# Performance work log

Measured on AMD Instinct MI355X. Metric: run time of the kernel, lower is better.

## Reference

```python
import jax, jax.numpy as jnp
import numpy as np
import math

HEADS = 16
D = 1024
HEAD_DIM = D // HEADS
SEQ = 2048
BATCH = 4
LN_EPS = 1e-5


def setup_inputs() -> dict:
    key = jax.random.key(0)
    ks = jax.random.split(key, 7)
    s = 1.0 / math.sqrt(HEAD_DIM)
    return {
        "q": jax.random.normal(ks[0], (SEQ, BATCH, D), dtype=jnp.float32),
        "k": jax.random.normal(ks[1], (SEQ, BATCH, D), dtype=jnp.float32),
        "v": jax.random.normal(ks[2], (SEQ, BATCH, D), dtype=jnp.float32),
        "Wq": jax.random.normal(ks[3], (HEAD_DIM, HEAD_DIM), dtype=jnp.float32) * s,
        "Wk": jax.random.normal(ks[4], (HEAD_DIM, HEAD_DIM), dtype=jnp.float32) * s,
        "Wv": jax.random.normal(ks[5], (HEAD_DIM, HEAD_DIM), dtype=jnp.float32) * s,
        "Wl": jax.random.normal(ks[6], (D, D), dtype=jnp.float32) * (1.0 / math.sqrt(D)),
        "gamma": jnp.ones((D,), dtype=jnp.float32),
        "beta": jnp.zeros((D,), dtype=jnp.float32),
    }


def reference(q, k, v, Wq, Wk, Wv, Wl, gamma, beta):
    # q, k, v: [seq_len, batch, d]  (seq-first, as in the torch module)
    q_len, batch = q.shape[0], q.shape[1]
    k_len, v_len = k.shape[0], v.shape[0]
    # Faithful to torch: reshape (NOT transpose) seq-first tensor into
    # (batch, len, heads, head_dim), then per-head linear (x @ W.T, no bias).
    Qh = jnp.einsum('bqhd,ed->bqhe', q.reshape(batch, q_len, HEADS, HEAD_DIM), Wq)
    Kh = jnp.einsum('bkhd,ed->bkhe', k.reshape(batch, k_len, HEADS, HEAD_DIM), Wk)
    Vh = jnp.einsum('bvhd,ed->bvhe', v.reshape(batch, v_len, HEADS, HEAD_DIM), Wv)
    # Scores scaled by sqrt(d) (full model dim), as in the original.
    scores = jnp.einsum('bqhd,bkhd->bhqk', Qh, Kh) / math.sqrt(D)
    attn = jax.nn.softmax(scores, axis=-1)  # dropout p=0.0 -> identity
    out = jnp.einsum('bhqk,bkhd->bqhd', attn, Vh)  # [b, q, h, d]
    concat = out.reshape(q_len, batch, D)
    lin = concat @ Wl.T
    mean = jnp.mean(lin, axis=-1, keepdims=True)
    var = jnp.var(lin, axis=-1, keepdims=True)
    ln = (lin - mean) * jax.lax.rsqrt(var + LN_EPS) * gamma + beta
    return q + ln
```

## Files before the change

kernel.cpp:

```cpp
#include <hip/hip_runtime.h>

#define LOG2E 1.4426950408889634f

typedef __attribute__((ext_vector_type(8))) short short8_t;
typedef __attribute__((ext_vector_type(4))) float floatx4;
typedef __attribute__((ext_vector_type(16))) float floatx16;

#define MFMA(a,b,c)   __builtin_amdgcn_mfma_f32_16x16x32_bf16(a,b,c,0,0,0)
#define MFMA32(a,b,c) __builtin_amdgcn_mfma_f32_32x32x16_bf16(a,b,c,0,0,0)
#define GLOAD(g, l) __builtin_amdgcn_global_load_lds( \
    (const __attribute__((address_space(1))) unsigned int*)(g), \
    (__attribute__((address_space(3))) unsigned int*)(l), 16, 0, 0)

__device__ __forceinline__ unsigned short f2bf(float f){
    unsigned u = __float_as_uint(f);
    u = u + 0x7FFFu + ((u >> 16) & 1u);
    return (unsigned short)(u >> 16);
}
__device__ __forceinline__ float bf2f(unsigned short s){
    return __uint_as_float(((unsigned)s) << 16);
}
__device__ __forceinline__ unsigned cvtpk(float lo, float hi){
    unsigned r;
    asm("v_cvt_pk_bf16_f32 %0, %1, %2" : "=v"(r) : "v"(lo), "v"(hi));
    return r;
}
__device__ __forceinline__ void plswap(unsigned &a, unsigned &b){
    asm volatile("v_permlane32_swap_b32 %0, %1" : "+v"(a), "+v"(b));
}

union U8 { unsigned u[4]; short8_t s8; };

__global__ __launch_bounds__(256) void proj_kernel(
    const float* __restrict__ Xq, const float* __restrict__ Xk, const float* __restrict__ Xv,
    const float* __restrict__ Wq, const float* __restrict__ Wk, const float* __restrict__ Wv,
    unsigned short* __restrict__ qp, unsigned short* __restrict__ kp, unsigned short* __restrict__ vp)
{
    const int rt = blockIdx.x;
    const int h  = blockIdx.y;
    const int sel= blockIdx.z;
    const float* X = (sel==0)?Xq:(sel==1)?Xk:Xv;
    const float* W = (sel==0)?Wq:(sel==1)?Wk:Wv;
    unsigned short* O = (sel==0)?qp:(sel==1)?kp:vp;
    const float qs = (sel==0) ? ((1.0f/32.0f)*LOG2E) : 1.0f;

    const int t  = threadIdx.x;
    const int w  = t >> 6, l = t & 63;
    const int r5 = l & 31;
    const int hf = l >> 5;

    const int row0 = rt*128 + w*32;

    short8_t a[4];
    {
        const float* xb = X + (size_t)(row0 + r5)*1024 + h*64 + hf*8;
        #pragma unroll
        for (int kb=0; kb<4; kb++){
            float4 f0 = *reinterpret_cast<const float4*>(xb + kb*16);
            float4 f1 = *reinterpret_cast<const float4*>(xb + kb*16 + 4);
            U8 u;
            u.u[0] = cvtpk(f0.x, f0.y); u.u[1] = cvtpk(f0.z, f0.w);
            u.u[2] = cvtpk(f1.x, f1.y); u.u[3] = cvtpk(f1.z, f1.w);
            a[kb] = u.s8;
        }
    }
    short8_t b[2][4];
    #pragma unroll
    for (int nb=0; nb<2; nb++){
        const float* wb = W + (size_t)(nb*32 + r5)*64 + hf*8;
        #pragma unroll
        for (int kb=0; kb<4; kb++){
            float4 f0 = *reinterpret_cast<const float4*>(wb + kb*16);
            float4 f1 = *reinterpret_cast<const float4*>(wb + kb*16 + 4);
            U8 u;
            u.u[0] = cvtpk(f0.x, f0.y); u.u[1] = cvtpk(f0.z, f0.w);
            u.u[2] = cvtpk(f1.x, f1.y); u.u[3] = cvtpk(f1.z, f1.w);
            b[nb][kb] = u.s8;
        }
    }

    floatx16 acc[2] = {};
    #pragma unroll
    for (int nb=0; nb<2; nb++)
        #pragma unroll
        for (int kb=0; kb<4; kb++)
            acc[nb] = MFMA32(a[kb], b[nb][kb], acc[nb]);

    const int c   = rt >> 4;
    const size_t chbase = (size_t)(c*16 + h);

    #pragma unroll
    for (int nb=0; nb<2; nb++){
        const int e = nb*32 + r5;
        #pragma unroll
        for (int m=0; m<4; m++){
            unsigned p01 = cvtpk(acc[nb][4*m]*qs,   acc[nb][4*m+1]*qs);
            unsigned p23 = cvtpk(acc[nb][4*m+2]*qs, acc[nb][4*m+3]*qs);
            #pragma unroll
            for (int i=0; i<4; i++){
                unsigned short val = (unsigned short)
                    ((i==0)?p01 : (i==1)?(p01>>16) : (i==2)?p23 : (p23>>16));
                const int gr = row0 + i + 8*m + 4*hf;
                const int s  = gr & 2047;
                size_t addr;
                if (sel == 0){
                    addr = (chbase*2048 + s)*64 + e;
                } else {
                    const int kt_ = s >> 6, rl = s & 63;
                    const size_t tbase = (chbase*32 + kt_)*4096;
                    if (sel == 1)
                        addr = tbase + rl*64 + (((e>>3) ^ (rl&7))<<3) + (e&7);
                    else
                        addr = tbase + e*64 + (((rl>>3) ^ (e&7))<<3) + (rl&7);
                }
                O[addr] = val;
            }
        }
    }
}

__global__ __launch_bounds__(256) void attn_kernel(
    const unsigned short* __restrict__ qp, const unsigned short* __restrict__ kp,
    const unsigned short* __restrict__ vp, unsigned short* __restrict__ ob)
{
    const int qt = blockIdx.x;
    const int hd = blockIdx.y;
    const int c  = blockIdx.z;
    const int t  = threadIdx.x;
    const int w  = t >> 6, l = t & 63;
    const int r5 = l & 31;
    const int hf = l >> 5;

    __shared__ unsigned short Ks[2][64][64];
    __shared__ unsigned short Vs[2][64][64];

    const size_t chq = ((size_t)(c*16 + hd))*2048*64;
    const size_t cht = ((size_t)(c*16 + hd))*32*4096;

    short8_t aq[4];
    {
        const unsigned short* qrow = qp + chq + (size_t)(qt*128 + w*32 + r5)*64 + hf*8;
        #pragma unroll
        for (int kb=0;kb<4;kb++)
            aq[kb] = *reinterpret_cast<const short8_t*>(qrow + kb*16);
    }

    const char* kbase = (const char*)(kp + cht) + w*2048 + l*16;
    const char* vbase = (const char*)(vp + cht) + w*2048 + l*16;
    char* kdst = (char*)(&Ks[0][0][0]) + w*2048;
    char* vdst = (char*)(&Vs[0][0][0]) + w*2048;

    #define ATTN_STAGE(buf, kt) do { \
        const char* ks_ = kbase + (size_t)(kt)*8192; \
        const char* vs_ = vbase + (size_t)(kt)*8192; \
        char* kd_ = kdst + (buf)*8192; \
        char* vd_ = vdst + (buf)*8192; \
        GLOAD(ks_,      kd_);      GLOAD(ks_+1024, kd_+1024); \
        GLOAD(vs_,      vd_);      GLOAD(vs_+1024, vd_+1024); \
    } while(0)

    const int x7 = r5 & 7;

    floatx16 oa[2] = {};
    float ls = 0.f;

    ATTN_STAGE(0, 0);

    for (int kt=0; kt<32; kt++){
        const int cur = kt & 1;
        if (kt < 31){
            ATTN_STAGE(cur^1, kt+1);
            asm volatile("s_waitcnt vmcnt(4)" ::: "memory");
        } else {
            asm volatile("s_waitcnt vmcnt(0)" ::: "memory");
        }
        __builtin_amdgcn_s_barrier();
        __builtin_amdgcn_sched_barrier(0);

        const unsigned short* Kc = &Ks[cur][0][0];
        const unsigned short* Vc = &Vs[cur][0][0];

        floatx16 sacc[2] = {};
        __builtin_amdgcn_s_setprio(1);
        #pragma unroll
        for (int mb=0;mb<2;mb++){
            #pragma unroll
            for (int kb=0;kb<4;kb++){
                short8_t kf = *reinterpret_cast<const short8_t*>(
                    Kc + (mb*32 + r5)*64 + (((kb*2 + hf) ^ x7)<<3));
                sacc[mb] = MFMA32(kf, aq[kb], sacc[mb]);
            }
        }
        __builtin_amdgcn_s_setprio(0);

        #pragma unroll
        for (int mb=0;mb<2;mb++)
            #pragma unroll
            for (int i=0;i<16;i++)
                sacc[mb][i] = __builtin_amdgcn_exp2f(sacc[mb][i]);

        float rsx[16];
        #pragma unroll
        for (int i=0;i<16;i++) rsx[i] = sacc[0][i] + sacc[1][i];
        #pragma unroll
        for (int s=8;s>0;s>>=1){
            #pragma unroll
            for (int i=0;i<s;i++) rsx[i] += rsx[i+s];
        }
        ls += rsx[0];

        short8_t F[4];
        #pragma unroll
        for (int mb=0;mb<2;mb++){
            unsigned lo[4], hi[4];
            #pragma unroll
            for (int m=0;m<4;m++){
                lo[m] = cvtpk(sacc[mb][4*m],   sacc[mb][4*m+1]);
                hi[m] = cvtpk(sacc[mb][4*m+2], sacc[mb][4*m+3]);
            }
            #pragma unroll
            for (int hk=0;hk<2;hk++){
                unsigned a = lo[2*hk], b = lo[2*hk+1];
                unsigned cc = hi[2*hk], d = hi[2*hk+1];
                plswap(a, b);
                plswap(cc, d);
                U8 fu;
                fu.u[0] = a; fu.u[1] = cc; fu.u[2] = b; fu.u[3] = d;
                F[mb*2 + hk] = fu.s8;
            }
        }

        __builtin_amdgcn_s_setprio(1);
        #pragma unroll
        for (int db=0;db<2;db++){
            #pragma unroll
            for (int kb2=0;kb2<4;kb2++){
                short8_t vf = *reinterpret_cast<const short8_t*>(
                    Vc + (db*32 + r5)*64 + (((kb2*2 + hf) ^ x7)<<3));
                oa[db] = MFMA32(vf, F[kb2], oa[db]);
            }
        }
        __builtin_amdgcn_s_setprio(0);

        __builtin_amdgcn_sched_barrier(0);
        __builtin_amdgcn_s_barrier();
    }

    ls += __shfl_xor(ls, 32);
    const float inv = 1.0f / ls;
    const size_t grow = (size_t)c*2048 + qt*128 + w*32 + r5;
    unsigned short* obp = ob + grow*1024 + hd*64 + hf*4;
    #pragma unroll
    for (int db=0;db<2;db++){
        #pragma unroll
        for (int m=0;m<4;m++){
            ushort4 u;
            u.x = f2bf(oa[db][4*m]*inv);   u.y = f2bf(oa[db][4*m+1]*inv);
            u.z = f2bf(oa[db][4*m+2]*inv); u.w = f2bf(oa[db][4*m+3]*inv);
            *reinterpret_cast<ushort4*>(obp + db*32 + m*8) = u;
        }
    }
}

__global__ __launch_bounds__(256) void wlconv_kernel(const float* __restrict__ W,
                                                     unsigned short* __restrict__ O)
{
    int i = (blockIdx.x*256 + threadIdx.x)*4;
    float4 f = *reinterpret_cast<const float4*>(W + i);
    ushort4 u;
    u.x = f2bf(f.x); u.y = f2bf(f.y); u.z = f2bf(f.z); u.w = f2bf(f.w);
    *reinterpret_cast<ushort4*>(O + i) = u;
}

__global__ __launch_bounds__(256) void gemm_kernel(
    const unsigned short* __restrict__ A, const unsigned short* __restrict__ B,
    unsigned short* __restrict__ C)
{
    const int bm = blockIdx.x, bn = blockIdx.y;
    __shared__ unsigned short As[2][128][64];
    __shared__ unsigned short Bs[2][128][64];
    const int t = threadIdx.x, w = t>>6, l = t&63;
    const int l15 = l&15, l4 = l>>4;
    const int wm = w>>1, wn = w&1;

    const char* asrc = (const char*)A + ((size_t)(bm*128 + w*32 + (l>>3)))*2048 + (l&7)*16;
    const char* bsrc = (const char*)B + ((size_t)(bn*128 + w*32 + (l>>3)))*2048 + (l&7)*16;
    char* adst = (char*)(&As[0][0][0]) + w*4096;
    char* bdst = (char*)(&Bs[0][0][0]) + w*4096;

    #define GEMM_STAGE(buf, kt) do { \
        const char* as_ = asrc + (size_t)(kt)*128; \
        const char* bs_ = bsrc + (size_t)(kt)*128; \
        char* ad_ = adst + (buf)*16384; \
        char* bd_ = bdst + (buf)*16384; \
        GLOAD(as_,          ad_);        GLOAD(as_+16384,  ad_+1024); \
        GLOAD(as_+32768,    ad_+2048);   GLOAD(as_+49152,  ad_+3072); \
        GLOAD(bs_,          bd_);        GLOAD(bs_+16384,  bd_+1024); \
        GLOAD(bs_+32768,    bd_+2048);   GLOAD(bs_+49152,  bd_+3072); \
    } while(0)

    floatx4 acc[4][4] = {};

    GEMM_STAGE(0, 0);

    for (int kt=0; kt<16; kt++){
        const int cur = kt & 1;
        if (kt < 15){
            GEMM_STAGE(cur^1, kt+1);
            asm volatile("s_waitcnt vmcnt(8)" ::: "memory");
        } else {
            asm volatile("s_waitcnt vmcnt(0)" ::: "memory");
        }
        __builtin_amdgcn_s_barrier();
        __builtin_amdgcn_sched_barrier(0);

        #pragma unroll
        for (int kk=0;kk<2;kk++){
            short8_t a[4], b[4];
            #pragma unroll
            for (int mt=0;mt<4;mt++)
                a[mt] = *reinterpret_cast<const short8_t*>(&As[cur][wm*64 + mt*16 + l15][kk*32 + l4*8]);
            #pragma unroll
            for (int nt=0;nt<4;nt++)
                b[nt] = *reinterpret_cast<const short8_t*>(&Bs[cur][wn*64 + nt*16 + l15][kk*32 + l4*8]);
            __builtin_amdgcn_s_setprio(1);
            #pragma unroll
            for (int mt=0;mt<4;mt++)
                #pragma unroll
                for (int nt=0;nt<4;nt++)
                    acc[mt][nt] = MFMA(a[mt], b[nt], acc[mt][nt]);
            __builtin_amdgcn_s_setprio(0);
        }

        __builtin_amdgcn_sched_barrier(0);
        __builtin_amdgcn_s_barrier();
    }

    #pragma unroll
    for (int mt=0;mt<4;mt++)
        #pragma unroll
        for (int nt=0;nt<4;nt++)
            #pragma unroll
            for (int j=0;j<4;j++){
                int row = bm*128 + wm*64 + mt*16 + l4*4 + j;
                int col = bn*128 + wn*64 + nt*16 + l15;
                C[(size_t)row*1024 + col] = f2bf(acc[mt][nt][j]);
            }
}

__global__ __launch_bounds__(256) void ln_kernel(
    const unsigned short* __restrict__ lin, const float* __restrict__ qin,
    const float* __restrict__ gamma, const float* __restrict__ beta, float* __restrict__ out)
{
    const int r = blockIdx.x, t = threadIdx.x;
    const unsigned short* row = lin + (size_t)r*1024;
    uint2 u = *reinterpret_cast<const uint2*>(row + t*4);
    float v0 = bf2f((unsigned short)(u.x & 0xffffu));
    float v1 = bf2f((unsigned short)(u.x >> 16));
    float v2 = bf2f((unsigned short)(u.y & 0xffffu));
    float v3 = bf2f((unsigned short)(u.y >> 16));
    float s  = v0+v1+v2+v3;
    float sq = v0*v0+v1*v1+v2*v2+v3*v3;
    #pragma unroll
    for (int d=1; d<64; d<<=1){ s += __shfl_xor(s, d); sq += __shfl_xor(sq, d); }
    __shared__ float red[8];
    if ((t&63)==0){ red[(t>>6)*2] = s; red[(t>>6)*2+1] = sq; }
    __syncthreads();
    s  = red[0]+red[2]+red[4]+red[6];
    sq = red[1]+red[3]+red[5]+red[7];
    float mean = s*(1.f/1024.f);
    float var  = sq*(1.f/1024.f) - mean*mean;
    float rs   = rsqrtf(var + 1e-5f);
    int base = r*1024 + t*4;
    float4 qv = *reinterpret_cast<const float4*>(qin + base);
    float4 g  = *reinterpret_cast<const float4*>(gamma + t*4);
    float4 b  = *reinterpret_cast<const float4*>(beta + t*4);
    float4 o;
    o.x = qv.x + (v0-mean)*rs*g.x + b.x;
    o.y = qv.y + (v1-mean)*rs*g.y + b.y;
    o.z = qv.z + (v2-mean)*rs*g.z + b.z;
    o.w = qv.w + (v3-mean)*rs*g.w + b.w;
    *reinterpret_cast<float4*>(out + base) = o;
}

extern "C" void kernel_launch(void* const* d_in, const int* in_sizes, int n_in,
                              void* d_out, int out_size, void* d_ws, size_t ws_size,
                              hipStream_t stream)
{
    (void)in_sizes; (void)n_in; (void)out_size; (void)ws_size;
    const float* q     = (const float*)d_in[0];
    const float* k     = (const float*)d_in[1];
    const float* v     = (const float*)d_in[2];
    const float* Wq    = (const float*)d_in[3];
    const float* Wk    = (const float*)d_in[4];
    const float* Wv    = (const float*)d_in[5];
    const float* Wl    = (const float*)d_in[6];
    const float* gamma = (const float*)d_in[7];
    const float* beta  = (const float*)d_in[8];
    float* out = (float*)d_out;

    char* ws = (char*)d_ws;
    unsigned short* qp  = (unsigned short*)(ws);
    unsigned short* kp  = (unsigned short*)(ws + (16u<<20));
    unsigned short* vp  = (unsigned short*)(ws + (32u<<20));
    unsigned short* ob  = (unsigned short*)(ws + (48u<<20));
    unsigned short* lin = (unsigned short*)(ws);
    unsigned short* wlb = (unsigned short*)(ws + (16u<<20));

    proj_kernel <<<dim3(64,16,3),  256, 0, stream>>>(q,k,v, Wq,Wk,Wv, qp,kp,vp);
    attn_kernel <<<dim3(16,16,4),  256, 0, stream>>>(qp,kp,vp, ob);
    wlconv_kernel<<<dim3(1024),    256, 0, stream>>>(Wl, wlb);
    gemm_kernel <<<dim3(64,8),     256, 0, stream>>>(ob, wlb, lin);
    ln_kernel   <<<dim3(8192),     256, 0, stream>>>(lin, q, gamma, beta, out);
}
```

Baseline: 190.9 us.

## Process two query tiles per wave in attention and compute row sums via MFMA

Each attention wave now handles 64 query rows (two 32-row tiles) instead of 32, so every K/V fragment read from LDS feeds two MFMAs. The grid is halved to match. The softmax row-sum is now accumulated with an MFMA against a vector of bf16 ones instead of a VALU reduction tree. This raises register pressure (launch bounds set to 1 block) and halves the block count, which may reduce occupancy and latency hiding.

```diff
diff --git a/kernel.cpp b/kernel.cpp
--- a/kernel.cpp
+++ b/kernel.cpp
@@ -119,7 +119,7 @@
     }
 }
 
-__global__ __launch_bounds__(256) void attn_kernel(
+__global__ __launch_bounds__(256,1) void attn_kernel(
     const unsigned short* __restrict__ qp, const unsigned short* __restrict__ kp,
     const unsigned short* __restrict__ vp, unsigned short* __restrict__ ob)
 {
@@ -137,12 +137,15 @@
     const size_t chq = ((size_t)(c*16 + hd))*2048*64;
     const size_t cht = ((size_t)(c*16 + hd))*32*4096;
 
-    short8_t aq[4];
+    short8_t aqA[4], aqB[4];
     {
-        const unsigned short* qrow = qp + chq + (size_t)(qt*128 + w*32 + r5)*64 + hf*8;
-        #pragma unroll
-        for (int kb=0;kb<4;kb++)
-            aq[kb] = *reinterpret_cast<const short8_t*>(qrow + kb*16);
+        const unsigned short* qrowA = qp + chq + (size_t)(qt*256 + w*64 + r5)*64 + hf*8;
+        const unsigned short* qrowB = qrowA + 32*64;
+        #pragma unroll
+        for (int kb=0;kb<4;kb++){
+            aqA[kb] = *reinterpret_cast<const short8_t*>(qrowA + kb*16);
+            aqB[kb] = *reinterpret_cast<const short8_t*>(qrowB + kb*16);
+        }
     }
 
     const char* kbase = (const char*)(kp + cht) + w*2048 + l*16;
@@ -161,8 +164,13 @@
 
     const int x7 = r5 & 7;
 
-    floatx16 oa[2] = {};
-    float ls = 0.f;
+    U8 onesu;
+    onesu.u[0] = 0x3F803F80u; onesu.u[1] = 0x3F803F80u;
+    onesu.u[2] = 0x3F803F80u; onesu.u[3] = 0x3F803F80u;
+    const short8_t ones8 = onesu.s8;
+
+    floatx16 oaA[2] = {}, oaB[2] = {};
+    floatx16 lsA = {}, lsB = {};
 
     ATTN_STAGE(0, 0);
 
@@ -180,7 +188,7 @@
         const unsigned short* Kc = &Ks[cur][0][0];
         const unsigned short* Vc = &Vs[cur][0][0];
 
-        floatx16 sacc[2] = {};
+        floatx16 sA[2] = {}, sB[2] = {};
         __builtin_amdgcn_s_setprio(1);
         #pragma unroll
         for (int mb=0;mb<2;mb++){
@@ -188,35 +196,26 @@
             for (int kb=0;kb<4;kb++){
                 short8_t kf = *reinterpret_cast<const short8_t*>(
                     Kc + (mb*32 + r5)*64 + (((kb*2 + hf) ^ x7)<<3));
-                sacc[mb] = MFMA32(kf, aq[kb], sacc[mb]);
+                sA[mb] = MFMA32(kf, aqA[kb], sA[mb]);
+                sB[mb] = MFMA32(kf, aqB[kb], sB[mb]);
             }
         }
         __builtin_amdgcn_s_setprio(0);
 
+        short8_t FA[4], FB[4];
+
         #pragma unroll
         for (int mb=0;mb<2;mb++)
             #pragma unroll
             for (int i=0;i<16;i++)
-                sacc[mb][i] = __builtin_amdgcn_exp2f(sacc[mb][i]);
-
-        float rsx[16];
-        #pragma unroll
-        for (int i=0;i<16;i++) rsx[i] = sacc[0][i] + sacc[1][i];
-        #pragma unroll
-        for (int s=8;s>0;s>>=1){
-            #pragma unroll
-            for (int i=0;i<s;i++) rsx[i] += rsx[i+s];
-        }
-        ls += rsx[0];
-
-        short8_t F[4];
+                sA[mb][i] = __builtin_amdgcn_exp2f(sA[mb][i]);
         #pragma unroll
         for (int mb=0;mb<2;mb++){
             unsigned lo[4], hi[4];
             #pragma unroll
             for (int m=0;m<4;m++){
-                lo[m] = cvtpk(sacc[mb][4*m],   sacc[mb][4*m+1]);
-                hi[m] = cvtpk(sacc[mb][4*m+2], sacc[mb][4*m+3]);
+                lo[m] = cvtpk(sA[mb][4*m],   sA[mb][4*m+1]);
+                hi[m] = cvtpk(sA[mb][4*m+2], sA[mb][4*m+3]);
             }
             #pragma unroll
             for (int hk=0;hk<2;hk++){
@@ -226,9 +225,38 @@
                 plswap(cc, d);
                 U8 fu;
                 fu.u[0] = a; fu.u[1] = cc; fu.u[2] = b; fu.u[3] = d;
-                F[mb*2 + hk] = fu.s8;
-            }
-        }
+                FA[mb*2 + hk] = fu.s8;
+            }
+        }
+        #pragma unroll
+        for (int f=0;f<4;f++) lsA = MFMA32(ones8, FA[f], lsA);
+
+        #pragma unroll
+        for (int mb=0;mb<2;mb++)
+            #pragma unroll
+            for (int i=0;i<16;i++)
+                sB[mb][i] = __builtin_amdgcn_exp2f(sB[mb][i]);
+        #pragma unroll
+        for (int mb=0;mb<2;mb++){
+            unsigned lo[4], hi[4];
+            #pragma unroll
+            for (int m=0;m<4;m++){
+                lo[m] = cvtpk(sB[mb][4*m],   sB[mb][4*m+1]);
+                hi[m] = cvtpk(sB[mb][4*m+2], sB[mb][4*m+3]);
+            }
+            #pragma unroll
+            for (int hk=0;hk<2;hk++){
+                unsigned a = lo[2*hk], b = lo[2*hk+1];
+                unsigned cc = hi[2*hk], d = hi[2*hk+1];
+                plswap(a, b);
+                plswap(cc, d);
+                U8 fu;
+                fu.u[0] = a; fu.u[1] = cc; fu.u[2] = b; fu.u[3] = d;
+                FB[mb*2 + hk] = fu.s8;
+            }
+        }
+        #pragma unroll
+        for (int f=0;f<4;f++) lsB = MFMA32(ones8, FB[f], lsB);
 
         __builtin_amdgcn_s_setprio(1);
         #pragma unroll
@@ -237,7 +265,8 @@
             for (int kb2=0;kb2<4;kb2++){
                 short8_t vf = *reinterpret_cast<const short8_t*>(
                     Vc + (db*32 + r5)*64 + (((kb2*2 + hf) ^ x7)<<3));
-                oa[db] = MFMA32(vf, F[kb2], oa[db]);
+                oaA[db] = MFMA32(vf, FA[kb2], oaA[db]);
+                oaB[db] = MFMA32(vf, FB[kb2], oaB[db]);
             }
         }
         __builtin_amdgcn_s_setprio(0);
@@ -246,18 +275,22 @@
         __builtin_amdgcn_s_barrier();
     }
 
-    ls += __shfl_xor(ls, 32);
-    const float inv = 1.0f / ls;
-    const size_t grow = (size_t)c*2048 + qt*128 + w*32 + r5;
-    unsigned short* obp = ob + grow*1024 + hd*64 + hf*4;
+    const float invA = 1.0f / lsA[0];
+    const float invB = 1.0f / lsB[0];
+    const size_t growA = (size_t)c*2048 + qt*256 + w*64 + r5;
+    unsigned short* obpA = ob + growA*1024 + hd*64 + hf*4;
+    unsigned short* obpB = obpA + (size_t)32*1024;
     #pragma unroll
     for (int db=0;db<2;db++){
         #pragma unroll
         for (int m=0;m<4;m++){
-            ushort4 u;
-            u.x = f2bf(oa[db][4*m]*inv);   u.y = f2bf(oa[db][4*m+1]*inv);
-            u.z = f2bf(oa[db][4*m+2]*inv); u.w = f2bf(oa[db][4*m+3]*inv);
-            *reinterpret_cast<ushort4*>(obp + db*32 + m*8) = u;
+            ushort4 uA, uB;
+            uA.x = f2bf(oaA[db][4*m]*invA);   uA.y = f2bf(oaA[db][4*m+1]*invA);
+            uA.z = f2bf(oaA[db][4*m+2]*invA); uA.w = f2bf(oaA[db][4*m+3]*invA);
+            uB.x = f2bf(oaB[db][4*m]*invB);   uB.y = f2bf(oaB[db][4*m+1]*invB);
+            uB.z = f2bf(oaB[db][4*m+2]*invB); uB.w = f2bf(oaB[db][4*m+3]*invB);
+            *reinterpret_cast<ushort4*>(obpA + db*32 + m*8) = uA;
+            *reinterpret_cast<ushort4*>(obpB + db*32 + m*8) = uB;
         }
     }
 }
@@ -408,7 +441,7 @@
     unsigned short* wlb = (unsigned short*)(ws + (16u<<20));
 
     proj_kernel <<<dim3(64,16,3),  256, 0, stream>>>(q,k,v, Wq,Wk,Wv, qp,kp,vp);
-    attn_kernel <<<dim3(16,16,4),  256, 0, stream>>>(qp,kp,vp, ob);
+    attn_kernel <<<dim3(8,16,4),   256, 0, stream>>>(qp,kp,vp, ob);
     wlconv_kernel<<<dim3(1024),    256, 0, stream>>>(Wl, wlb);
     gemm_kernel <<<dim3(64,8),     256, 0, stream>>>(ob, wlb, lin);
     ln_kernel   <<<dim3(8192),     256, 0, stream>>>(lin, q, gamma, beta, out);
```

New measurement: 209.4 us. 1.1x slower.

## Compute softmax row sums via MFMA with ones and swizzle attention block order

Applied to the files above, without the earlier changes.

Replaces the per-thread VALU reduction of exponentiated scores with four extra MFMA instructions that multiply a bf16 ones vector by the probability fragments, accumulating row sums in a matrix register. This takes the sum off the vector ALU, which competes with exp2 and packing, at the cost of extra matrix work. The sums now use the bf16-rounded probabilities, so they match what is multiplied with V. The 3D grid becomes a 1D grid with a swizzled mapping that spreads head/batch pairs across XCDs so K/V tiles are shared in each XCD's L2, and launch bounds now declare one block per CU.

```diff
diff --git a/kernel.cpp b/kernel.cpp
--- a/kernel.cpp
+++ b/kernel.cpp
@@ -119,13 +119,18 @@
     }
 }
 
-__global__ __launch_bounds__(256) void attn_kernel(
+__global__ __launch_bounds__(256,1) void attn_kernel(
     const unsigned short* __restrict__ qp, const unsigned short* __restrict__ kp,
     const unsigned short* __restrict__ vp, unsigned short* __restrict__ ob)
 {
-    const int qt = blockIdx.x;
-    const int hd = blockIdx.y;
-    const int c  = blockIdx.z;
+    const int bswz = blockIdx.x;
+    const int xr   = bswz & 7;
+    const int rest = bswz >> 3;
+    const int qt   = rest & 15;
+    const int p    = xr + 8*(rest >> 4);
+    const int hd   = p & 15;
+    const int c    = p >> 4;
+
     const int t  = threadIdx.x;
     const int w  = t >> 6, l = t & 63;
     const int r5 = l & 31;
@@ -161,8 +166,13 @@
 
     const int x7 = r5 & 7;
 
+    U8 onesu;
+    onesu.u[0] = 0x3F803F80u; onesu.u[1] = 0x3F803F80u;
+    onesu.u[2] = 0x3F803F80u; onesu.u[3] = 0x3F803F80u;
+    const short8_t ones8 = onesu.s8;
+
     floatx16 oa[2] = {};
-    float ls = 0.f;
+    floatx16 lsv = {};
 
     ATTN_STAGE(0, 0);
 
@@ -198,16 +208,6 @@
             #pragma unroll
             for (int i=0;i<16;i++)
                 sacc[mb][i] = __builtin_amdgcn_exp2f(sacc[mb][i]);
-
-        float rsx[16];
-        #pragma unroll
-        for (int i=0;i<16;i++) rsx[i] = sacc[0][i] + sacc[1][i];
-        #pragma unroll
-        for (int s=8;s>0;s>>=1){
-            #pragma unroll
-            for (int i=0;i<s;i++) rsx[i] += rsx[i+s];
-        }
-        ls += rsx[0];
 
         short8_t F[4];
         #pragma unroll
@@ -232,6 +232,8 @@
 
         __builtin_amdgcn_s_setprio(1);
         #pragma unroll
+        for (int f=0;f<4;f++) lsv = MFMA32(ones8, F[f], lsv);
+        #pragma unroll
         for (int db=0;db<2;db++){
             #pragma unroll
             for (int kb2=0;kb2<4;kb2++){
@@ -246,8 +248,7 @@
         __builtin_amdgcn_s_barrier();
     }
 
-    ls += __shfl_xor(ls, 32);
-    const float inv = 1.0f / ls;
+    const float inv = 1.0f / lsv[0];
     const size_t grow = (size_t)c*2048 + qt*128 + w*32 + r5;
     unsigned short* obp = ob + grow*1024 + hd*64 + hf*4;
     #pragma unroll
@@ -408,7 +409,7 @@
     unsigned short* wlb = (unsigned short*)(ws + (16u<<20));
 
     proj_kernel <<<dim3(64,16,3),  256, 0, stream>>>(q,k,v, Wq,Wk,Wv, qp,kp,vp);
-    attn_kernel <<<dim3(16,16,4),  256, 0, stream>>>(qp,kp,vp, ob);
+    attn_kernel <<<dim3(1024),     256, 0, stream>>>(qp,kp,vp, ob);
     wlconv_kernel<<<dim3(1024),    256, 0, stream>>>(Wl, wlb);
     gemm_kernel <<<dim3(64,8),     256, 0, stream>>>(ob, wlb, lin);
     ln_kernel   <<<dim3(8192),     256, 0, stream>>>(lin, q, gamma, beta, out);
```

Result: faster. 185.8 us (-2.7%).
